# Kernel tuning notes

Measured on AMD Instinct MI355X. Metric: run time of the kernel, lower is better.

The kernel has to match this reference:

```python
import jax, jax.numpy as jnp
import numpy as np
from functools import partial

DT = 0.1
EPS_RES = 0.01
EIG_MIN = 0.1
EIG_CLIP = 0.99
CHUNK = 128

B, T, D, K = 8, 4096, 1024, 256


def setup_inputs() -> dict:
    key = jax.random.key(0)
    k1, k2, k3, k4, k5 = jax.random.split(key, 5)
    x = jax.random.normal(k1, (B, T, D), dtype=jnp.float32)
    # paper init: alpha ~ U(-3, 0)
    alpha_raw = -3.0 * jax.random.uniform(k2, (K,), dtype=jnp.float32)
    # omega_k = 2*pi*k/K
    omega = 2.0 * jnp.pi * jnp.arange(K, dtype=jnp.float32) / K
    W_in = jax.random.normal(k3, (K, D), dtype=jnp.float32) / np.sqrt(D)
    W_out = jax.random.normal(k4, (D, K), dtype=jnp.float32) / np.sqrt(K)
    M = jax.random.normal(k5, (K, K), dtype=jnp.float32)
    return {"x": x, "alpha_raw": alpha_raw, "omega": omega,
            "W_in": W_in, "W_out": W_out, "M": M}


def _forward(x, alpha_raw, omega, W_in, W_out, M):
    Bb, Tt, Dd = x.shape
    Kk = alpha_raw.shape[0]
    n_chunks = Tt // CHUNK

    # eigenvalue magnitude/phase with constraints
    mag = EIG_MIN + jax.nn.sigmoid(alpha_raw) * (EIG_CLIP - EIG_MIN)     # (K,)
    cos_p = jnp.cos(omega * DT)
    sin_p = jnp.sin(omega * DT)
    # resonance R = I + eps * M / ||M||_F
    R = jnp.eye(Kk, dtype=x.dtype) + EPS_RES * M / (jnp.linalg.norm(M) + 1e-8)

    # parallel input projection for all timesteps: (B,T,K)
    beta = jnp.einsum('btd,kd->btk', x, W_in)
    # (n_chunks, CHUNK, B, K) for scanning over chunks then timesteps
    beta_c = jnp.transpose(beta.reshape(Bb, n_chunks, CHUNK, Kk), (1, 2, 0, 3))

    def time_step(carry, b):
        r, i = carry                                     # (B,K) each
        nr = b + mag * (r * cos_p - i * sin_p)           # beta added to real only
        ni = mag * (r * sin_p + i * cos_p)
        return (nr, ni), (nr, ni)

    def chunk_step(carry, beta_ch):
        # beta_ch: (CHUNK, B, K)
        (_, _), (ar, ai) = jax.lax.scan(time_step, carry, beta_ch)
        # resonance coupling applied to every state of the chunk
        ar = ar @ R
        ai = ai @ R
        # state handed to next chunk is the resonance-coupled last state,
        # detached at the chunk boundary (as in the original training scheme)
        new_carry = (jax.lax.stop_gradient(ar[-1]), jax.lax.stop_gradient(ai[-1]))
        return new_carry, ar

    zero = jnp.zeros((Bb, Kk), dtype=x.dtype)
    _, states_real = jax.lax.scan(chunk_step, (zero, zero), beta_c)
    # states_real: (n_chunks, CHUNK, B, K) -> (B, T, K)
    states_real = jnp.transpose(states_real, (2, 0, 1, 3)).reshape(Bb, Tt, Kk)

    # parallel output projection (dropout is identity in eval)
    out = jnp.einsum('btk,dk->btd', states_real, W_out)
    return out


@jax.jit
def reference(x, alpha_raw, omega, W_in, W_out, M):
    return _forward(x, alpha_raw, omega, W_in, W_out, M)
```

## Files before the change

### kernel.cpp

```cpp
#include <hip/hip_runtime.h>
#include <math.h>


typedef __attribute__((ext_vector_type(8))) short short8;
typedef __attribute__((ext_vector_type(4))) float f32x4;

#define EPS_RES 0.01f

union U8 { unsigned u[4]; short8 s8; };

__device__ __forceinline__ unsigned short f2bf(float f) {
  unsigned u = __float_as_uint(f) + 0x8000u;
  return (unsigned short)(u >> 16);
}
__device__ __forceinline__ float bf2f(unsigned short h) {
  return __uint_as_float(((unsigned)h) << 16);
}
__device__ __forceinline__ unsigned pk2bf(float f0, float f1) {
  return __builtin_amdgcn_perm(__float_as_uint(f1) + 0x8000u,
                               __float_as_uint(f0) + 0x8000u, 0x07060302u);
}
__device__ __forceinline__ void gl_lds16(const void* g, void* l) {
  __builtin_amdgcn_global_load_lds(
      (const __attribute__((address_space(1))) unsigned*)g,
      (__attribute__((address_space(3))) unsigned*)l, 16, 0, 0);
}

__global__ __launch_bounds__(256) void k_norm1(const float* __restrict__ M,
                                               float* __restrict__ part) {
  const int i = (blockIdx.x * 256 + threadIdx.x) * 4;
  const float4 v = *(const float4*)(M + i);
  float s = v.x * v.x + v.y * v.y + v.z * v.z + v.w * v.w;
  #pragma unroll
  for (int off = 32; off > 0; off >>= 1) s += __shfl_down(s, off);
  __shared__ float red[4];
  const int lane = threadIdx.x & 63, wv = threadIdx.x >> 6;
  if (lane == 0) red[wv] = s;
  __syncthreads();
  if (threadIdx.x == 0)
    part[blockIdx.x] = red[0] + red[1] + red[2] + red[3];
}

__global__ __launch_bounds__(64) void k_norm2(const float* __restrict__ part,
                                              float* __restrict__ norm_out) {
  float s = part[threadIdx.x];
  #pragma unroll
  for (int off = 32; off > 0; off >>= 1) s += __shfl_down(s, off);
  if (threadIdx.x == 0) norm_out[0] = sqrtf(s);
}

__global__ __launch_bounds__(256) void k_prep(const float* __restrict__ W,
                                              unsigned short* __restrict__ o) {
  const int i = (blockIdx.x * 256 + threadIdx.x) * 4;
  float4 v = *(const float4*)(W + i);
  uint2 p;
  p.x = pk2bf(v.x, v.y);
  p.y = pk2bf(v.z, v.w);
  *(uint2*)(o + i) = p;
}

__global__ __launch_bounds__(256) void k_wcomb(const float* __restrict__ Wout,
                                               const float* __restrict__ Mm,
                                               const float* __restrict__ normp,
                                               unsigned short* __restrict__ WcT) {
  const int d0 = blockIdx.x * 8;
  const int k = threadIdx.x;
  __shared__ float wl[8][256];
  #pragma unroll
  for (int dd = 0; dd < 8; ++dd) wl[dd][k] = Wout[(size_t)(d0 + dd) * 256 + k];
  __syncthreads();
  float acc[8] = {0.f, 0.f, 0.f, 0.f, 0.f, 0.f, 0.f, 0.f};
  const float4* Mr = (const float4*)(Mm + (size_t)k * 256);
  for (int j4 = 0; j4 < 64; ++j4) {
    const float4 m4 = Mr[j4];
    #pragma unroll
    for (int dd = 0; dd < 8; ++dd) {
      acc[dd] = fmaf(m4.x, wl[dd][j4 * 4 + 0], acc[dd]);
      acc[dd] = fmaf(m4.y, wl[dd][j4 * 4 + 1], acc[dd]);
      acc[dd] = fmaf(m4.z, wl[dd][j4 * 4 + 2], acc[dd]);
      acc[dd] = fmaf(m4.w, wl[dd][j4 * 4 + 3], acc[dd]);
    }
  }
  const float s = EPS_RES / (normp[0] + 1e-8f);
  #pragma unroll
  for (int dd = 0; dd < 8; ++dd)
    WcT[(size_t)(d0 + dd) * 256 + k] =
        f2bf(Wout[(size_t)(d0 + dd) * 256 + k] + s * acc[dd]);
}

__global__ __launch_bounds__(256) void k_gemm1(const float* __restrict__ A,
                                               const unsigned short* __restrict__ Bw,
                                               float* __restrict__ C) {
  __shared__ __align__(16) float lA[2][64 * 32];
  __shared__ __align__(16) unsigned short lB[2][256 * 32];
  const int tid = threadIdx.x;
  const int wv = tid >> 6, lane = tid & 63;
  const int m0 = blockIdx.x * 64;
  const int wn = wv;
  const int lrow = lane & 15, q = lane >> 4;

  const int a_r8 = lane >> 3;
  const int a_gl = (lane & 7) ^ a_r8;
  const int b_r16 = lane >> 2;
  const int b_gl = (lane & 3) ^ ((b_r16 >> 1) & 3);

  const float* Ab = A + (size_t)(m0 + wv * 16 + a_r8) * 1024 + a_gl * 4;
  const unsigned short* Bb = Bw + (size_t)(wv * 64 + b_r16) * 1024 + b_gl * 8;

  f32x4 acc[4][4] = {};

  auto stage = [&](int bf, int k0) {
    #pragma unroll
    for (int j = 0; j < 2; ++j)
      gl_lds16(Ab + (size_t)j * 8 * 1024 + k0,
               &lA[bf][(wv * 16 + j * 8) * 32]);
    #pragma unroll
    for (int j = 0; j < 4; ++j)
      gl_lds16(Bb + (size_t)j * 16 * 1024 + k0,
               &lB[bf][(wv * 64 + j * 16) * 32]);
  };

  stage(0, 0);
  for (int s32 = 0; s32 < 32; ++s32) {
    const int cur = s32 & 1;
    __syncthreads();
    if (s32 + 1 < 32) stage(cur ^ 1, (s32 + 1) * 32);

    short8 af[4], bfv[4];
    #pragma unroll
    for (int t = 0; t < 4; ++t) {
      const int ra = t * 16 + lrow, sw = ra & 7;
      const float4 lo = *(const float4*)&lA[cur][ra * 32 + (((2 * q) ^ sw) << 2)];
      const float4 hi = *(const float4*)&lA[cur][ra * 32 + (((2 * q + 1) ^ sw) << 2)];
      U8 u;
      u.u[0] = pk2bf(lo.x, lo.y);
      u.u[1] = pk2bf(lo.z, lo.w);
      u.u[2] = pk2bf(hi.x, hi.y);
      u.u[3] = pk2bf(hi.z, hi.w);
      af[t] = u.s8;
      const int rb = wn * 64 + t * 16 + lrow;
      bfv[t] = *(const short8*)&lB[cur][rb * 32 + (q ^ ((rb >> 1) & 3)) * 8];
    }
    #pragma unroll
    for (int tm = 0; tm < 4; ++tm)
      #pragma unroll
      for (int tn = 0; tn < 4; ++tn)
        acc[tm][tn] = __builtin_amdgcn_mfma_f32_16x16x32_bf16(
            af[tm], bfv[tn], acc[tm][tn], 0, 0, 0);
  }

  const int rbase = m0 + q * 4;
  const int cbase = wn * 64 + lrow;
  #pragma unroll
  for (int tm = 0; tm < 4; ++tm)
    #pragma unroll
    for (int tn = 0; tn < 4; ++tn)
      #pragma unroll
      for (int r = 0; r < 4; ++r)
        C[(size_t)(rbase + tm * 16 + r) * 256 + (cbase + tn * 16)] =
            acc[tm][tn][r];
}

__global__ __launch_bounds__(256) void k_gemm2(const unsigned short* __restrict__ A,
                                               const unsigned short* __restrict__ Bw,
                                               float* __restrict__ C) {
  __shared__ __align__(16) unsigned short lA[2][128 * 64];
  __shared__ __align__(16) unsigned short lB[2][128 * 64];
  const int tid = threadIdx.x;
  const int wv = tid >> 6, lane = tid & 63;
  const int bid = blockIdx.x + (blockIdx.y << 8);
  const int xcd = bid & 7, ii = bid >> 3;
  const int m0 = ((xcd << 5) + (ii >> 3)) * 128;
  const int n0 = (ii & 7) * 128;
  const int wm = wv & 1, wn = wv >> 1;
  const int lrow = lane & 15, q = lane >> 4;

  const int r8 = lane >> 3;
  const int gl = (lane & 7) ^ r8;

  const unsigned short* Ab = A + (size_t)(m0 + wv * 32 + r8) * 256 + gl * 8;
  const unsigned short* Bb = Bw + (size_t)(n0 + wv * 32 + r8) * 256 + gl * 8;

  f32x4 acc[4][4] = {};

  auto stage = [&](int bf, int k0) {
    #pragma unroll
    for (int j = 0; j < 4; ++j) {
      gl_lds16(Ab + (size_t)j * 8 * 256 + k0, &lA[bf][(wv * 32 + j * 8) * 64]);
      gl_lds16(Bb + (size_t)j * 8 * 256 + k0, &lB[bf][(wv * 32 + j * 8) * 64]);
    }
  };

  stage(0, 0);
  for (int s64 = 0; s64 < 4; ++s64) {
    const int cur = s64 & 1;
    __syncthreads();
    if (s64 + 1 < 4) stage(cur ^ 1, (s64 + 1) * 64);

    #pragma unroll
    for (int ks = 0; ks < 2; ++ks) {
      short8 af[4], bfv[4];
      #pragma unroll
      for (int t = 0; t < 4; ++t) {
        const int ra = wm * 64 + t * 16 + lrow;
        af[t] = *(const short8*)
            &lA[cur][ra * 64 + (((ks * 4 + q) ^ (ra & 7)) << 3)];
        const int rb = wn * 64 + t * 16 + lrow;
        bfv[t] = *(const short8*)
            &lB[cur][rb * 64 + (((ks * 4 + q) ^ (rb & 7)) << 3)];
      }
      #pragma unroll
      for (int tm = 0; tm < 4; ++tm)
        #pragma unroll
        for (int tn = 0; tn < 4; ++tn)
          acc[tm][tn] = __builtin_amdgcn_mfma_f32_16x16x32_bf16(
              af[tm], bfv[tn], acc[tm][tn], 0, 0, 0);
    }
  }

  const int rbase = m0 + wm * 64 + (lane >> 4) * 4;
  const int cbase = n0 + wn * 64 + (lane & 15);
  #pragma unroll
  for (int tm = 0; tm < 4; ++tm)
    #pragma unroll
    for (int tn = 0; tn < 4; ++tn)
      #pragma unroll
      for (int r = 0; r < 4; ++r)
        C[(size_t)(rbase + tm * 16 + r) * 1024 + (cbase + tn * 16)] =
            acc[tm][tn][r];
}

__global__ __launch_bounds__(256) void k_scan(const float* __restrict__ beta,
                                              unsigned short* __restrict__ rez,
                                              float* __restrict__ lastR,
                                              float* __restrict__ lastI,
                                              const float* __restrict__ alpha_raw,
                                              const float* __restrict__ omega) {
  const int c = blockIdx.x & 31, b = blockIdx.x >> 5;
  const int k = threadIdx.x;
  const float a = alpha_raw[k];
  const float sig = 1.f / (1.f + expf(-a));
  const float mag = 0.1f + sig * (0.99f - 0.1f);
  const float om = omega[k] * 0.1f;
  const float lc = mag * cosf(om), ls = mag * sinf(om);

  const size_t m0 = (size_t)b * 4096 + (size_t)c * 128;
  const float* bp = beta + m0 * 256 + k;
  unsigned short* rp = rez + m0 * 256 + k;
  float r = 0.f, im = 0.f;
  #pragma unroll 8
  for (int t = 0; t < 128; ++t) {
    float be = bp[(size_t)t * 256];
    float nr = fmaf(lc, r, fmaf(-ls, im, be));
    float ni = fmaf(ls, r, lc * im);
    r = nr; im = ni;
    rp[(size_t)t * 256] = f2bf(r);
  }
  const int idx = (c * 8 + b) * 256 + k;
  lastR[idx] = r;
  lastI[idx] = im;
}

__global__ __launch_bounds__(256) void k_carry(const float* __restrict__ lastR,
                                               const float* __restrict__ lastI,
                                               const float* __restrict__ Mm,
                                               const float* __restrict__ normp,
                                               float* __restrict__ carR,
                                               float* __restrict__ carI) {
  const int c = blockIdx.x & 31, b = blockIdx.x >> 5;
  const int j = threadIdx.x;
  const int oidx = (c * 8 + b) * 256 + j;
  if (c == 0) {
    carR[oidx] = 0.f;
    carI[oidx] = 0.f;
    return;
  }
  __shared__ float lr[256], li[256];
  const int iidx = ((c - 1) * 8 + b) * 256;
  lr[j] = lastR[iidx + j];
  li[j] = lastI[iidx + j];
  __syncthreads();
  float ar = 0.f, ai = 0.f;
  for (int kk = 0; kk < 256; ++kk) {
    float m = Mm[(size_t)kk * 256 + j];
    ar = fmaf(lr[kk], m, ar);
    ai = fmaf(li[kk], m, ai);
  }
  const float s = EPS_RES / (normp[0] + 1e-8f);
  carR[oidx] = lr[j] + s * ar;
  carI[oidx] = li[j] + s * ai;
}

__global__ __launch_bounds__(256) void k_fixup(unsigned short* __restrict__ rez,
                                               const float* __restrict__ carR,
                                               const float* __restrict__ carI,
                                               const float* __restrict__ alpha_raw,
                                               const float* __restrict__ omega) {
  const int tg = blockIdx.x & 7;
  const int cb = blockIdx.x >> 3;
  const int b = cb & 7, c = (cb >> 3) + 1;
  const int k = threadIdx.x;
  const float a = alpha_raw[k];
  const float sig = 1.f / (1.f + expf(-a));
  const float mag = 0.1f + sig * (0.99f - 0.1f);
  const float om = omega[k] * 0.1f;
  const float l2m = log2f(mag);

  const float cr = carR[(c * 8 + b) * 256 + k];
  const float ci = carI[(c * 8 + b) * 256 + k];
  unsigned short* rp =
      rez + ((size_t)b * 4096 + (size_t)c * 128 + tg * 8) * 256 + k;
  #pragma unroll
  for (int tt = 0; tt < 8; ++tt) {
    const float tp1 = (float)(tg * 8 + tt + 1);
    const float p = exp2f(tp1 * l2m);
    const float ang = tp1 * om;
    const float hr = p * (cosf(ang) * cr - sinf(ang) * ci);
    rp[(size_t)tt * 256] = f2bf(bf2f(rp[(size_t)tt * 256]) + hr);
  }
}

extern "C" void kernel_launch(void* const* d_in, const int* in_sizes, int n_in,
                              void* d_out, int out_size, void* d_ws,
                              size_t ws_size, hipStream_t stream) {
  const float* x         = (const float*)d_in[0];
  const float* alpha_raw = (const float*)d_in[1];
  const float* omega     = (const float*)d_in[2];
  const float* W_in      = (const float*)d_in[3];
  const float* W_out     = (const float*)d_in[4];
  const float* Mm        = (const float*)d_in[5];
  float* out = (float*)d_out;

  char* ws = (char*)d_ws;
  float*          beta  = (float*)(ws);
  unsigned short* rez   = (unsigned short*)(ws + 33554432);
  float*          lastR = (float*)(ws + 50331648);
  float*          lastI = (float*)(ws + 50331648 + 262144);
  float*          carR  = (float*)(ws + 50331648 + 2 * 262144);
  float*          carI  = (float*)(ws + 50331648 + 3 * 262144);
  unsigned short* WcT   = (unsigned short*)(ws + 50331648 + 4 * 262144);
  float*          normp = (float*)(ws + 50331648 + 4 * 262144 + 524288);
  float*          npart = (float*)(ws + 50331648 + 4 * 262144 + 524288 + 256);
  unsigned short* WinT  = (unsigned short*)d_out;

  k_norm1<<<64, 256, 0, stream>>>(Mm, npart);
  k_norm2<<<1, 64, 0, stream>>>(npart, normp);
  k_wcomb<<<128, 256, 0, stream>>>(W_out, Mm, normp, WcT);
  k_prep<<<256, 256, 0, stream>>>(W_in, WinT);
  k_gemm1<<<512, 256, 0, stream>>>(x, WinT, beta);
  k_scan<<<256, 256, 0, stream>>>(beta, rez, lastR, lastI, alpha_raw, omega);
  k_carry<<<256, 256, 0, stream>>>(lastR, lastI, Mm, normp, carR, carI);
  k_fixup<<<1984, 256, 0, stream>>>(rez, carR, carI, alpha_raw, omega);
  k_gemm2<<<dim3(256, 8), 256, 0, stream>>>(rez, WcT, out);
}
```

Before: 336.4 us.

## Triple-buffer GEMM loads with vmcnt waits and merge setup kernels

Both GEMM kernels move from double-buffered LDS staging with __syncthreads to a three-stage ring. Explicit s_waitcnt vmcnt lets two tiles stay in flight while the current one is computed. gemm2 also shrinks its K-tile from 64 to 32 with a new swizzle so the extra buffer fits in LDS. The norm and W_in bf16 conversion kernels are merged into one launch, and the final norm reduction is recomputed inside the consumer kernels instead of running a separate single-block kernel. This cuts launch count and exposed load latency, at the cost of more LDS, more barriers in gemm2, and hand-counted vmcnt values that must match the number of issued loads.

```diff
diff --git a/kernel.cpp b/kernel.cpp
--- a/kernel.cpp
+++ b/kernel.cpp
@@ -26,42 +26,43 @@
       (__attribute__((address_space(3))) unsigned*)l, 16, 0, 0);
 }
 
-__global__ __launch_bounds__(256) void k_norm1(const float* __restrict__ M,
-                                               float* __restrict__ part) {
-  const int i = (blockIdx.x * 256 + threadIdx.x) * 4;
-  const float4 v = *(const float4*)(M + i);
-  float s = v.x * v.x + v.y * v.y + v.z * v.z + v.w * v.w;
-  #pragma unroll
-  for (int off = 32; off > 0; off >>= 1) s += __shfl_down(s, off);
-  __shared__ float red[4];
-  const int lane = threadIdx.x & 63, wv = threadIdx.x >> 6;
-  if (lane == 0) red[wv] = s;
-  __syncthreads();
-  if (threadIdx.x == 0)
-    part[blockIdx.x] = red[0] + red[1] + red[2] + red[3];
-}
-
-__global__ __launch_bounds__(64) void k_norm2(const float* __restrict__ part,
-                                              float* __restrict__ norm_out) {
-  float s = part[threadIdx.x];
-  #pragma unroll
-  for (int off = 32; off > 0; off >>= 1) s += __shfl_down(s, off);
-  if (threadIdx.x == 0) norm_out[0] = sqrtf(s);
-}
-
-__global__ __launch_bounds__(256) void k_prep(const float* __restrict__ W,
-                                              unsigned short* __restrict__ o) {
-  const int i = (blockIdx.x * 256 + threadIdx.x) * 4;
-  float4 v = *(const float4*)(W + i);
-  uint2 p;
-  p.x = pk2bf(v.x, v.y);
-  p.y = pk2bf(v.z, v.w);
-  *(uint2*)(o + i) = p;
+__global__ __launch_bounds__(256) void k_setup(const float* __restrict__ M,
+                                               float* __restrict__ part,
+                                               const float* __restrict__ W,
+                                               unsigned short* __restrict__ o) {
+  const int bid = blockIdx.x;
+  if (bid < 64) {
+    const int i = (bid * 256 + threadIdx.x) * 4;
+    const float4 v = *(const float4*)(M + i);
+    float s = v.x * v.x + v.y * v.y + v.z * v.z + v.w * v.w;
+    #pragma unroll
+    for (int off = 32; off > 0; off >>= 1) s += __shfl_down(s, off);
+    __shared__ float red[4];
+    const int lane = threadIdx.x & 63, wv = threadIdx.x >> 6;
+    if (lane == 0) red[wv] = s;
+    __syncthreads();
+    if (threadIdx.x == 0)
+      part[bid] = red[0] + red[1] + red[2] + red[3];
+  } else {
+    const int i = ((bid - 64) * 256 + threadIdx.x) * 4;
+    float4 v = *(const float4*)(W + i);
+    uint2 p;
+    p.x = pk2bf(v.x, v.y);
+    p.y = pk2bf(v.z, v.w);
+    *(uint2*)(o + i) = p;
+  }
+}
+
+__device__ __forceinline__ float norm_scale(const float* __restrict__ part) {
+  float nsum = 0.f;
+  #pragma unroll
+  for (int i = 0; i < 64; ++i) nsum += part[i];
+  return EPS_RES / (sqrtf(nsum) + 1e-8f);
 }
 
 __global__ __launch_bounds__(256) void k_wcomb(const float* __restrict__ Wout,
                                                const float* __restrict__ Mm,
-                                               const float* __restrict__ normp,
+                                               const float* __restrict__ npart,
                                                unsigned short* __restrict__ WcT) {
   const int d0 = blockIdx.x * 8;
   const int k = threadIdx.x;
@@ -81,7 +82,7 @@
       acc[dd] = fmaf(m4.w, wl[dd][j4 * 4 + 3], acc[dd]);
     }
   }
-  const float s = EPS_RES / (normp[0] + 1e-8f);
+  const float s = norm_scale(npart);
   #pragma unroll
   for (int dd = 0; dd < 8; ++dd)
     WcT[(size_t)(d0 + dd) * 256 + k] =
@@ -91,8 +92,8 @@
 __global__ __launch_bounds__(256) void k_gemm1(const float* __restrict__ A,
                                                const unsigned short* __restrict__ Bw,
                                                float* __restrict__ C) {
-  __shared__ __align__(16) float lA[2][64 * 32];
-  __shared__ __align__(16) unsigned short lB[2][256 * 32];
+  __shared__ __align__(16) float lA[3][64 * 32];
+  __shared__ __align__(16) unsigned short lB[3][256 * 32];
   const int tid = threadIdx.x;
   const int wv = tid >> 6, lane = tid & 63;
   const int m0 = blockIdx.x * 64;
@@ -120,12 +121,7 @@
                &lB[bf][(wv * 64 + j * 16) * 32]);
   };
 
-  stage(0, 0);
-  for (int s32 = 0; s32 < 32; ++s32) {
-    const int cur = s32 & 1;
-    __syncthreads();
-    if (s32 + 1 < 32) stage(cur ^ 1, (s32 + 1) * 32);
-
+  auto compute = [&](int cur) {
     short8 af[4], bfv[4];
     #pragma unroll
     for (int t = 0; t < 4; ++t) {
@@ -147,7 +143,24 @@
       for (int tn = 0; tn < 4; ++tn)
         acc[tm][tn] = __builtin_amdgcn_mfma_f32_16x16x32_bf16(
             af[tm], bfv[tn], acc[tm][tn], 0, 0, 0);
-  }
+  };
+
+  stage(0, 0);
+  stage(1, 32);
+  int cur = 0;
+  for (int j = 0; j < 31; ++j) {
+    asm volatile("s_waitcnt vmcnt(6)" ::: "memory");
+    __builtin_amdgcn_s_barrier();
+    if (j + 2 < 32) {
+      const int nx = (cur + 2 >= 3) ? cur - 1 : cur + 2;
+      stage(nx, (j + 2) * 32);
+    }
+    compute(cur);
+    cur = (cur + 1 >= 3) ? 0 : cur + 1;
+  }
+  asm volatile("s_waitcnt vmcnt(0)" ::: "memory");
+  __builtin_amdgcn_s_barrier();
+  compute(cur);
 
   const int rbase = m0 + q * 4;
   const int cbase = wn * 64 + lrow;
@@ -164,8 +177,8 @@
 __global__ __launch_bounds__(256) void k_gemm2(const unsigned short* __restrict__ A,
                                                const unsigned short* __restrict__ Bw,
                                                float* __restrict__ C) {
-  __shared__ __align__(16) unsigned short lA[2][128 * 64];
-  __shared__ __align__(16) unsigned short lB[2][128 * 64];
+  __shared__ __align__(16) unsigned short lA[3][128 * 32];
+  __shared__ __align__(16) unsigned short lB[3][128 * 32];
   const int tid = threadIdx.x;
   const int wv = tid >> 6, lane = tid & 63;
   const int bid = blockIdx.x + (blockIdx.y << 8);
@@ -175,48 +188,57 @@
   const int wm = wv & 1, wn = wv >> 1;
   const int lrow = lane & 15, q = lane >> 4;
 
-  const int r8 = lane >> 3;
-  const int gl = (lane & 7) ^ r8;
-
-  const unsigned short* Ab = A + (size_t)(m0 + wv * 32 + r8) * 256 + gl * 8;
-  const unsigned short* Bb = Bw + (size_t)(n0 + wv * 32 + r8) * 256 + gl * 8;
+  const int r16 = lane >> 2;
+  const int g4 = (lane & 3) ^ ((r16 >> 1) & 3);
+
+  const unsigned short* Ab = A + (size_t)(m0 + wv * 32 + r16) * 256 + g4 * 8;
+  const unsigned short* Bb = Bw + (size_t)(n0 + wv * 32 + r16) * 256 + g4 * 8;
 
   f32x4 acc[4][4] = {};
 
   auto stage = [&](int bf, int k0) {
     #pragma unroll
-    for (int j = 0; j < 4; ++j) {
-      gl_lds16(Ab + (size_t)j * 8 * 256 + k0, &lA[bf][(wv * 32 + j * 8) * 64]);
-      gl_lds16(Bb + (size_t)j * 8 * 256 + k0, &lB[bf][(wv * 32 + j * 8) * 64]);
+    for (int j = 0; j < 2; ++j) {
+      gl_lds16(Ab + (size_t)j * 16 * 256 + k0,
+               &lA[bf][(wv * 32 + j * 16) * 32]);
+      gl_lds16(Bb + (size_t)j * 16 * 256 + k0,
+               &lB[bf][(wv * 32 + j * 16) * 32]);
     }
   };
 
+  auto compute = [&](int cur) {
+    short8 af[4], bfv[4];
+    #pragma unroll
+    for (int t = 0; t < 4; ++t) {
+      const int ra = wm * 64 + t * 16 + lrow;
+      af[t] = *(const short8*)&lA[cur][ra * 32 + ((q ^ ((ra >> 1) & 3)) << 3)];
+      const int rb = wn * 64 + t * 16 + lrow;
+      bfv[t] = *(const short8*)&lB[cur][rb * 32 + ((q ^ ((rb >> 1) & 3)) << 3)];
+    }
+    #pragma unroll
+    for (int tm = 0; tm < 4; ++tm)
+      #pragma unroll
+      for (int tn = 0; tn < 4; ++tn)
+        acc[tm][tn] = __builtin_amdgcn_mfma_f32_16x16x32_bf16(
+            af[tm], bfv[tn], acc[tm][tn], 0, 0, 0);
+  };
+
   stage(0, 0);
-  for (int s64 = 0; s64 < 4; ++s64) {
-    const int cur = s64 & 1;
-    __syncthreads();
-    if (s64 + 1 < 4) stage(cur ^ 1, (s64 + 1) * 64);
-
-    #pragma unroll
-    for (int ks = 0; ks < 2; ++ks) {
-      short8 af[4], bfv[4];
-      #pragma unroll
-      for (int t = 0; t < 4; ++t) {
-        const int ra = wm * 64 + t * 16 + lrow;
-        af[t] = *(const short8*)
-            &lA[cur][ra * 64 + (((ks * 4 + q) ^ (ra & 7)) << 3)];
-        const int rb = wn * 64 + t * 16 + lrow;
-        bfv[t] = *(const short8*)
-            &lB[cur][rb * 64 + (((ks * 4 + q) ^ (rb & 7)) << 3)];
-      }
-      #pragma unroll
-      for (int tm = 0; tm < 4; ++tm)
-        #pragma unroll
-        for (int tn = 0; tn < 4; ++tn)
-          acc[tm][tn] = __builtin_amdgcn_mfma_f32_16x16x32_bf16(
-              af[tm], bfv[tn], acc[tm][tn], 0, 0, 0);
-    }
-  }
+  stage(1, 32);
+  int cur = 0;
+  for (int j = 0; j < 7; ++j) {
+    asm volatile("s_waitcnt vmcnt(4)" ::: "memory");
+    __builtin_amdgcn_s_barrier();
+    if (j + 2 < 8) {
+      const int nx = (cur + 2 >= 3) ? cur - 1 : cur + 2;
+      stage(nx, (j + 2) * 32);
+    }
+    compute(cur);
+    cur = (cur + 1 >= 3) ? 0 : cur + 1;
+  }
+  asm volatile("s_waitcnt vmcnt(0)" ::: "memory");
+  __builtin_amdgcn_s_barrier();
+  compute(cur);
 
   const int rbase = m0 + wm * 64 + (lane >> 4) * 4;
   const int cbase = n0 + wn * 64 + (lane & 15);
@@ -264,7 +286,7 @@
 __global__ __launch_bounds__(256) void k_carry(const float* __restrict__ lastR,
                                                const float* __restrict__ lastI,
                                                const float* __restrict__ Mm,
-                                               const float* __restrict__ normp,
+                                               const float* __restrict__ npart,
                                                float* __restrict__ carR,
                                                float* __restrict__ carI) {
   const int c = blockIdx.x & 31, b = blockIdx.x >> 5;
@@ -286,7 +308,7 @@
     ar = fmaf(lr[kk], m, ar);
     ai = fmaf(li[kk], m, ai);
   }
-  const float s = EPS_RES / (normp[0] + 1e-8f);
+  const float s = norm_scale(npart);
   carR[oidx] = lr[j] + s * ar;
   carI[oidx] = li[j] + s * ai;
 }
@@ -339,17 +361,14 @@
   float*          carR  = (float*)(ws + 50331648 + 2 * 262144);
   float*          carI  = (float*)(ws + 50331648 + 3 * 262144);
   unsigned short* WcT   = (unsigned short*)(ws + 50331648 + 4 * 262144);
-  float*          normp = (float*)(ws + 50331648 + 4 * 262144 + 524288);
-  float*          npart = (float*)(ws + 50331648 + 4 * 262144 + 524288 + 256);
+  float*          npart = (float*)(ws + 50331648 + 4 * 262144 + 524288);
   unsigned short* WinT  = (unsigned short*)d_out;
 
-  k_norm1<<<64, 256, 0, stream>>>(Mm, npart);
-  k_norm2<<<1, 64, 0, stream>>>(npart, normp);
-  k_wcomb<<<128, 256, 0, stream>>>(W_out, Mm, normp, WcT);
-  k_prep<<<256, 256, 0, stream>>>(W_in, WinT);
+  k_setup<<<320, 256, 0, stream>>>(Mm, npart, W_in, WinT);
+  k_wcomb<<<128, 256, 0, stream>>>(W_out, Mm, npart, WcT);
   k_gemm1<<<512, 256, 0, stream>>>(x, WinT, beta);
   k_scan<<<256, 256, 0, stream>>>(beta, rez, lastR, lastI, alpha_raw, omega);
-  k_carry<<<256, 256, 0, stream>>>(lastR, lastI, Mm, normp, carR, carI);
+  k_carry<<<256, 256, 0, stream>>>(lastR, lastI, Mm, npart, carR, carI);
   k_fixup<<<1984, 256, 0, stream>>>(rez, carR, carI, alpha_raw, omega);
   k_gemm2<<<dim3(256, 8), 256, 0, stream>>>(rez, WcT, out);
 }
```

Measured after the change: 329.7 us. 2.0% less time.
